# Optimization experiments

Measured on AMD Instinct MI355X. Metric: run time of the kernel, lower is better.

## Reference

```python
import jax, jax.numpy as jnp
import numpy as np

N_NODES = 100000
N_EDGES = 1600000
IN_CH, HID_CH, OUT_CH = 128, 64, 32


def setup_inputs() -> dict:
    key = jax.random.key(0)
    k1, k2, k3, k4 = jax.random.split(key, 4)
    x = jax.random.normal(k1, (N_NODES, IN_CH), dtype=jnp.float32)
    edge_index = jax.random.randint(k2, (2, N_EDGES), 0, N_NODES, dtype=jnp.int32)
    # Glorot-ish scaling like PyG's GCNConv init
    W1 = jax.random.normal(k3, (IN_CH, HID_CH), dtype=jnp.float32) / np.sqrt(IN_CH)
    b1 = jnp.zeros((HID_CH,), dtype=jnp.float32)
    W2 = jax.random.normal(k4, (HID_CH, OUT_CH), dtype=jnp.float32) / np.sqrt(HID_CH)
    b2 = jnp.zeros((OUT_CH,), dtype=jnp.float32)
    return {"x": x, "edge_index": edge_index, "W1": W1, "b1": b1, "W2": W2, "b2": b2}


def reference(x, edge_index, W1, b1, W2, b2):
    # PyG GCNConv semantics: add self-loops, symmetric deg^{-1/2} normalization,
    # linear transform, scatter-add aggregation to destination nodes, add bias.
    N = x.shape[0]
    loops = jnp.arange(N, dtype=edge_index.dtype)
    src = jnp.concatenate([edge_index[0], loops])  # [E+N]
    dst = jnp.concatenate([edge_index[1], loops])  # [E+N]

    deg = jax.ops.segment_sum(jnp.ones_like(src, dtype=x.dtype), dst, num_segments=N)
    dis = jnp.where(deg > 0, jax.lax.rsqrt(jnp.maximum(deg, 1.0)), 0.0)  # deg^{-1/2}
    norm = (dis[src] * dis[dst])[:, None]  # [E+N, 1]

    def gcn_conv(h, W, b):
        h = h @ W                                   # [N, C_out]
        msgs = h[src] * norm                        # gather + scale, [E+N, C_out]
        return jax.ops.segment_sum(msgs, dst, num_segments=N) + b

    h = jax.nn.relu(gcn_conv(x, W1, b1))
    # dropout is identity in eval mode (training=False)
    return gcn_conv(h, W2, b2)
```

## Files before the change

kernel.cpp:

```cpp
#include <hip/hip_runtime.h>
#include <hip/hip_bf16.h>

#define IN_CH 128
#define HID_CH 64
#define OUT_CH 32
#define EPB 2048
#define MAXB 512

typedef unsigned short ushort_t;
typedef __attribute__((ext_vector_type(8))) short short8;
typedef __attribute__((ext_vector_type(4))) float float4v;

static __device__ __forceinline__ ushort_t f2bf(float f) {
    unsigned u = __float_as_uint(f);
    unsigned r = (u + 0x7fff + ((u >> 16) & 1)) >> 16;
    return (ushort_t)r;
}
static __device__ __forceinline__ float bf_lo(unsigned u) { return __uint_as_float(u << 16); }
static __device__ __forceinline__ float bf_hi(unsigned u) { return __uint_as_float(u & 0xffff0000u); }


__global__ __launch_bounds__(256) void k_partition(const int* __restrict__ src,
                                                   const int* __restrict__ dst,
                                                   int* __restrict__ gcursor,
                                                   unsigned* __restrict__ pairs,
                                                   int E, int nbk, int cap) {
    __shared__ int lhist[MAXB];
    __shared__ int lbase[MAXB];
    __shared__ int lcur[MAXB];
    const int tid = threadIdx.x;
    for (int b = tid; b < nbk; b += 256) { lhist[b] = 0; lcur[b] = 0; }
    __syncthreads();
    int s[8], d[8];
    const int e0 = blockIdx.x * EPB;
#pragma unroll
    for (int j = 0; j < 8; ++j) {
        int e = e0 + j * 256 + tid;
        if (e < E) {
            s[j] = src[e];
            d[j] = dst[e];
            atomicAdd(&lhist[d[j] >> 8], 1);
        } else {
            d[j] = -1;
        }
    }
    __syncthreads();
    for (int b = tid; b < nbk; b += 256)
        lbase[b] = lhist[b] ? atomicAdd(&gcursor[b], lhist[b]) : 0;
    __syncthreads();
#pragma unroll
    for (int j = 0; j < 8; ++j) {
        if (d[j] >= 0) {
            int b = d[j] >> 8;
            int loc = atomicAdd(&lcur[b], 1);
            int idx = lbase[b] + loc;
            if (idx < cap)
                pairs[(long long)b * cap + idx] = ((unsigned)s[j] << 8) | (unsigned)(d[j] & 255);
        }
    }
}

__global__ __launch_bounds__(512) void k_bscan(const int* __restrict__ gcursor,
                                               int* __restrict__ bbase,
                                               int* __restrict__ rowptr,
                                               int nbk, int cap, int N) {
    __shared__ int s[512];
    const int tid = threadIdx.x;
    int v = (tid < nbk) ? min(gcursor[tid], cap) : 0;
    s[tid] = v;
    __syncthreads();
    for (int off = 1; off < 512; off <<= 1) {
        int val = (tid >= off) ? s[tid - off] : 0;
        __syncthreads();
        s[tid] += val;
        __syncthreads();
    }
    if (tid < nbk) bbase[tid] = s[tid] - v;
    if (tid == nbk - 1) rowptr[N] = s[tid];
}

__global__ __launch_bounds__(256) void k_bucket_build(const unsigned* __restrict__ pairs,
                                                      const int* __restrict__ gcursor,
                                                      const int* __restrict__ bbase,
                                                      int* __restrict__ rowptr,
                                                      int* __restrict__ col,
                                                      float* __restrict__ dis,
                                                      int cap, int N) {
    __shared__ int lc[256];
    __shared__ int ls[256];
    __shared__ int lcur[256];
    const int b = blockIdx.x, tid = threadIdx.x;
    lc[tid] = 0;
    __syncthreads();
    const int cnt = min(gcursor[b], cap);
    const int base = bbase[b];
    const unsigned* p = pairs + (long long)b * cap;
    for (int i = tid; i < cnt; i += 256) atomicAdd(&lc[p[i] & 255], 1);
    __syncthreads();
    const int v = lc[tid];
    ls[tid] = v;
    __syncthreads();
    for (int off = 1; off < 256; off <<= 1) {
        int val = (tid >= off) ? ls[tid - off] : 0;
        __syncthreads();
        ls[tid] += val;
        __syncthreads();
    }
    const int excl = ls[tid] - v;
    const int row = b * 256 + tid;
    if (row < N) {
        rowptr[row] = base + excl;
        dis[row] = rsqrtf((float)(v + 1));
    }
    lcur[tid] = base + excl;
    __syncthreads();
    for (int i = tid; i < cnt; i += 256) {
        unsigned pk = p[i];
        int pos = atomicAdd(&lcur[pk & 255], 1);
        col[pos] = (int)(pk >> 8);
    }
}


__global__ __launch_bounds__(256) void k_prepW(const float* __restrict__ W,
                                               unsigned* __restrict__ wsW) {
    int s = blockIdx.x * 256 + threadIdx.x;
    if (s >= 1024) return;
    int lane = s & 63;
    int nt = (s >> 6) & 3;
    int kc = s >> 8;
    int c = nt * 16 + (lane & 15);
    int k0 = kc * 32 + (lane >> 4) * 8;
    unsigned o[4];
#pragma unroll
    for (int d = 0; d < 4; ++d) {
        unsigned lo = f2bf(W[(k0 + 2 * d) * 64 + c]);
        unsigned hi = f2bf(W[(k0 + 2 * d + 1) * 64 + c]);
        o[d] = lo | (hi << 16);
    }
    ((uint4*)wsW)[s] = make_uint4(o[0], o[1], o[2], o[3]);
}


__global__ __launch_bounds__(256) void k_mm1(const float* __restrict__ X,
                                             const unsigned* __restrict__ wsW,
                                             ushort_t* __restrict__ H, int N) {
    const int tid = threadIdx.x;
    const int wv = tid >> 6, lane = tid & 63;
    const int quad = lane >> 4, n16 = lane & 15;
    const int rowbase = blockIdx.x * 64 + wv * 16;
    const int myrow = rowbase + n16;
    const bool rok = (myrow < N);

    float4v acc0 = {}, acc1 = {}, acc2 = {}, acc3 = {};

#pragma unroll
    for (int kc = 0; kc < 4; ++kc) {
        float4 xa = make_float4(0.f, 0.f, 0.f, 0.f), xb = xa;
        if (rok) {
            const float4* p = (const float4*)(X + (long long)myrow * 128 + kc * 32 + quad * 8);
            xa = p[0];
            xb = p[1];
        }
        unsigned pk[4];
        pk[0] = (unsigned)f2bf(xa.x) | ((unsigned)f2bf(xa.y) << 16);
        pk[1] = (unsigned)f2bf(xa.z) | ((unsigned)f2bf(xa.w) << 16);
        pk[2] = (unsigned)f2bf(xb.x) | ((unsigned)f2bf(xb.y) << 16);
        pk[3] = (unsigned)f2bf(xb.z) | ((unsigned)f2bf(xb.w) << 16);
        short8 a;
        a[0] = (short)(pk[0] & 0xffff); a[1] = (short)(pk[0] >> 16);
        a[2] = (short)(pk[1] & 0xffff); a[3] = (short)(pk[1] >> 16);
        a[4] = (short)(pk[2] & 0xffff); a[5] = (short)(pk[2] >> 16);
        a[6] = (short)(pk[3] & 0xffff); a[7] = (short)(pk[3] >> 16);

        const short8* wb = (const short8*)wsW;
        short8 b0 = wb[(kc * 4 + 0) * 64 + lane];
        short8 b1 = wb[(kc * 4 + 1) * 64 + lane];
        short8 b2 = wb[(kc * 4 + 2) * 64 + lane];
        short8 b3 = wb[(kc * 4 + 3) * 64 + lane];

        acc0 = __builtin_amdgcn_mfma_f32_16x16x32_bf16(a, b0, acc0, 0, 0, 0);
        acc1 = __builtin_amdgcn_mfma_f32_16x16x32_bf16(a, b1, acc1, 0, 0, 0);
        acc2 = __builtin_amdgcn_mfma_f32_16x16x32_bf16(a, b2, acc2, 0, 0, 0);
        acc3 = __builtin_amdgcn_mfma_f32_16x16x32_bf16(a, b3, acc3, 0, 0, 0);
    }

#pragma unroll
    for (int i = 0; i < 4; ++i) {
        int row = rowbase + quad * 4 + i;
        if (row < N) {
            long long o = (long long)row * 64 + n16;
            H[o]      = f2bf(acc0[i]);
            H[o + 16] = f2bf(acc1[i]);
            H[o + 32] = f2bf(acc2[i]);
            H[o + 48] = f2bf(acc3[i]);
        }
    }
}


__global__ __launch_bounds__(256) void k_mm2(const unsigned* __restrict__ Z,
                                             const float* __restrict__ W,
                                             ushort_t* __restrict__ H, int N) {
    __shared__ float sW[64 * 32];
    __shared__ float sX[64 * 64];
    const int tid = threadIdx.x;
    for (int i = tid; i < 512; i += 256) ((float4*)sW)[i] = ((const float4*)W)[i];
    const long long row0 = (long long)blockIdx.x * 64;
    for (int i = tid; i < 2048; i += 256) {
        int r = i >> 5;
        int cp = i & 31;
        long long row = row0 + r;
        unsigned u = (row < N) ? Z[row * 32 + cp] : 0u;
        sX[r * 64 + 2 * cp]     = fmaxf(bf_lo(u), 0.f);
        sX[r * 64 + 2 * cp + 1] = fmaxf(bf_hi(u), 0.f);
    }
    __syncthreads();
    const int wv = tid >> 6, lane = tid & 63;
    const int c = lane & 31, hf = lane >> 5;
    const int rbase = wv * 16 + hf * 8;
    float acc[8] = {};
#pragma unroll 2
    for (int k = 0; k < 64; k += 4) {
        float4 xv[8];
#pragma unroll
        for (int r = 0; r < 8; ++r) xv[r] = *(const float4*)&sX[(rbase + r) * 64 + k];
        float w0 = sW[k * 32 + c];
        float w1 = sW[(k + 1) * 32 + c];
        float w2 = sW[(k + 2) * 32 + c];
        float w3 = sW[(k + 3) * 32 + c];
#pragma unroll
        for (int r = 0; r < 8; ++r)
            acc[r] += xv[r].x * w0 + xv[r].y * w1 + xv[r].z * w2 + xv[r].w * w3;
    }
#pragma unroll
    for (int r = 0; r < 8; ++r) {
        long long row = row0 + rbase + r;
        if (row < N) H[row * 32 + c] = f2bf(acc[r]);
    }
}


__global__ __launch_bounds__(256) void k_agg64(const unsigned* __restrict__ h,
                                               const int* __restrict__ rowptr,
                                               const int* __restrict__ col,
                                               const float* __restrict__ dis,
                                               const float* __restrict__ b,
                                               unsigned* __restrict__ z, int N) {
    const int wave = (blockIdx.x * 256 + threadIdx.x) >> 6;
    const int lane = threadIdx.x & 63;
    if (wave >= N) return;
    const int row = wave;
    const int t = lane & 31, g = lane >> 5;
    const int start = rowptr[row];
    const int deg = rowptr[row + 1] - start;
    const float dr = dis[row];

    int myCol = row;
    float myDis = 0.f;
    if (lane < deg) {
        myCol = col[start + lane];
        myDis = dis[myCol];
    }

    unsigned us = h[row * 32 + t];
    float w0s = g ? 0.f : dr;
    float ax = w0s * bf_lo(us), ay = w0s * bf_hi(us);

    const int cnt = min(deg, 64);
    for (int k0 = 0; k0 < cnt; k0 += 8) {
#pragma unroll
        for (int u = 0; u < 4; ++u) {
            int slot = k0 + 2 * u + g;
            int s = __shfl(myCol, slot);
            float w = __shfl(myDis, slot);
            unsigned uu = h[s * 32 + t];
            ax += w * bf_lo(uu);
            ay += w * bf_hi(uu);
        }
    }
    for (int j = start + 64 + g; j < start + deg; j += 2) {
        int s = col[j];
        float w = dis[s];
        unsigned uu = h[s * 32 + t];
        ax += w * bf_lo(uu);
        ay += w * bf_hi(uu);
    }
    ax += __shfl_down(ax, 32);
    ay += __shfl_down(ay, 32);
    if (!g) {
        float2 bv = ((const float2*)b)[t];
        float ox = bv.x + dr * ax;
        float oy = bv.y + dr * ay;
        z[row * 32 + t] = (unsigned)f2bf(ox) | ((unsigned)f2bf(oy) << 16);
    }
}

__global__ __launch_bounds__(256) void k_agg32(const unsigned* __restrict__ h,
                                               const int* __restrict__ rowptr,
                                               const int* __restrict__ col,
                                               const float* __restrict__ dis,
                                               const float* __restrict__ b,
                                               float* __restrict__ out, int N) {
    const int wave = (blockIdx.x * 256 + threadIdx.x) >> 6;
    const int lane = threadIdx.x & 63;
    if (wave >= N) return;
    const int row = wave;
    const int t = lane & 15, g = lane >> 4;
    const int start = rowptr[row];
    const int deg = rowptr[row + 1] - start;
    const float dr = dis[row];

    int myCol = row;
    float myDis = 0.f;
    if (lane < deg) {
        myCol = col[start + lane];
        myDis = dis[myCol];
    }

    unsigned us = h[row * 16 + t];
    float w0s = g ? 0.f : dr;
    float ax = w0s * bf_lo(us), ay = w0s * bf_hi(us);

    const int cnt = min(deg, 64);
    for (int k0 = 0; k0 < cnt; k0 += 16) {
#pragma unroll
        for (int u = 0; u < 4; ++u) {
            int slot = k0 + 4 * u + g;
            int s = __shfl(myCol, slot);
            float w = __shfl(myDis, slot);
            unsigned uu = h[s * 16 + t];
            ax += w * bf_lo(uu);
            ay += w * bf_hi(uu);
        }
    }
    for (int j = start + 64 + g; j < start + deg; j += 4) {
        int s = col[j];
        float w = dis[s];
        unsigned uu = h[s * 16 + t];
        ax += w * bf_lo(uu);
        ay += w * bf_hi(uu);
    }
    ax += __shfl_down(ax, 32);
    ay += __shfl_down(ay, 32);
    ax += __shfl_down(ax, 16);
    ay += __shfl_down(ay, 16);
    if (!g) {
        float2 bv = ((const float2*)b)[t];
        float2 o;
        o.x = bv.x + dr * ax;
        o.y = bv.y + dr * ay;
        ((float2*)out)[row * 16 + t] = o;
    }
}

extern "C" void kernel_launch(void* const* d_in, const int* in_sizes, int n_in,
                              void* d_out, int out_size, void* d_ws, size_t ws_size,
                              hipStream_t stream) {
    const float* x  = (const float*)d_in[0];
    const int*   ei = (const int*)d_in[1];
    const float* W1 = (const float*)d_in[2];
    const float* b1 = (const float*)d_in[3];
    const float* W2 = (const float*)d_in[4];
    const float* b2 = (const float*)d_in[5];
    float* out = (float*)d_out;

    const int N = in_sizes[0] / IN_CH;
    const int E = in_sizes[1] / 2;
    const int* esrc = ei;
    const int* edst = ei + E;

    int nbk = (N + 255) >> 8;
    if (nbk > MAXB) nbk = MAXB;
    const int per_b = (E + nbk - 1) / nbk;
    const int cap = per_b + per_b / 4 + 256;

    int* rowptr   = (int*)d_ws;
    int* gcursor  = rowptr + (((N + 1) + 15) & ~15);
    int* bbase    = gcursor + MAXB;
    unsigned* wsW = (unsigned*)(bbase + MAXB);
    int* col      = (int*)(wsW + 4096);
    float* dis    = (float*)(col + ((E + 15) & ~15));
    ushort_t* h1  = (ushort_t*)(dis + ((N + 15) & ~15));
    unsigned* z1  = (unsigned*)(h1 + (((long long)N * 64 + 31) & ~31LL));
    unsigned* pairs = z1;
    ushort_t* h2  = h1;

    const int B = 256;

    hipMemsetAsync(gcursor, 0, MAXB * sizeof(int), stream);
    k_prepW<<<4, B, 0, stream>>>(W1, wsW);
    k_partition<<<(E + EPB - 1) / EPB, B, 0, stream>>>(esrc, edst, gcursor, pairs, E, nbk, cap);
    k_bscan<<<1, 512, 0, stream>>>(gcursor, bbase, rowptr, nbk, cap, N);
    k_bucket_build<<<nbk, B, 0, stream>>>(pairs, gcursor, bbase, rowptr, col, dis, cap, N);

    k_mm1<<<(N + 63) / 64, B, 0, stream>>>(x, wsW, h1, N);
    k_agg64<<<((long long)N * 64 + B - 1) / B, B, 0, stream>>>((const unsigned*)h1, rowptr, col, dis, b1, z1, N);

    k_mm2<<<(N + 63) / 64, B, 0, stream>>>(z1, W2, h2, N);
    k_agg32<<<((long long)N * 64 + B - 1) / B, B, 0, stream>>>((const unsigned*)h2, rowptr, col, dis, b2, out, N);
}
```

Before: 261.5 us.

## Fuse layer-1 aggregation with second matmul and drop separate memset

Merges the 64-channel aggregation kernel with the 64x32 matmul: each wave aggregates a row, stages it in shared memory, applies ReLU and multiplies by W2 held in registers, then writes the bf16 32-channel row. This removes the intermediate z1 write/read and one kernel launch. The gcursor memset is folded into the weight prep kernel, and the gather loops in both aggregation kernels are unrolled further. The fused kernel uses a grid-stride loop with 8 rows per wave and keeps 32 weight registers per lane, which may raise register pressure and lower occupancy for the latency-bound gather.

```diff
diff --git a/kernel.cpp b/kernel.cpp
--- a/kernel.cpp
+++ b/kernel.cpp
@@ -123,8 +123,10 @@
 
 
 __global__ __launch_bounds__(256) void k_prepW(const float* __restrict__ W,
-                                               unsigned* __restrict__ wsW) {
+                                               unsigned* __restrict__ wsW,
+                                               int* __restrict__ gcursor) {
     int s = blockIdx.x * 256 + threadIdx.x;
+    if (s < MAXB) gcursor[s] = 0;
     if (s >= 1024) return;
     int lane = s & 63;
     int nt = (s >> 6) & 3;
@@ -199,102 +201,89 @@
 }
 
 
-__global__ __launch_bounds__(256) void k_mm2(const unsigned* __restrict__ Z,
-                                             const float* __restrict__ W,
-                                             ushort_t* __restrict__ H, int N) {
-    __shared__ float sW[64 * 32];
-    __shared__ float sX[64 * 64];
-    const int tid = threadIdx.x;
-    for (int i = tid; i < 512; i += 256) ((float4*)sW)[i] = ((const float4*)W)[i];
-    const long long row0 = (long long)blockIdx.x * 64;
-    for (int i = tid; i < 2048; i += 256) {
-        int r = i >> 5;
-        int cp = i & 31;
-        long long row = row0 + r;
-        unsigned u = (row < N) ? Z[row * 32 + cp] : 0u;
-        sX[r * 64 + 2 * cp]     = fmaxf(bf_lo(u), 0.f);
-        sX[r * 64 + 2 * cp + 1] = fmaxf(bf_hi(u), 0.f);
-    }
-    __syncthreads();
-    const int wv = tid >> 6, lane = tid & 63;
-    const int c = lane & 31, hf = lane >> 5;
-    const int rbase = wv * 16 + hf * 8;
-    float acc[8] = {};
-#pragma unroll 2
-    for (int k = 0; k < 64; k += 4) {
-        float4 xv[8];
-#pragma unroll
-        for (int r = 0; r < 8; ++r) xv[r] = *(const float4*)&sX[(rbase + r) * 64 + k];
-        float w0 = sW[k * 32 + c];
-        float w1 = sW[(k + 1) * 32 + c];
-        float w2 = sW[(k + 2) * 32 + c];
-        float w3 = sW[(k + 3) * 32 + c];
-#pragma unroll
-        for (int r = 0; r < 8; ++r)
-            acc[r] += xv[r].x * w0 + xv[r].y * w1 + xv[r].z * w2 + xv[r].w * w3;
-    }
-#pragma unroll
-    for (int r = 0; r < 8; ++r) {
-        long long row = row0 + rbase + r;
-        if (row < N) H[row * 32 + c] = f2bf(acc[r]);
-    }
-}
-
-
-__global__ __launch_bounds__(256) void k_agg64(const unsigned* __restrict__ h,
-                                               const int* __restrict__ rowptr,
-                                               const int* __restrict__ col,
-                                               const float* __restrict__ dis,
-                                               const float* __restrict__ b,
-                                               unsigned* __restrict__ z, int N) {
-    const int wave = (blockIdx.x * 256 + threadIdx.x) >> 6;
-    const int lane = threadIdx.x & 63;
-    if (wave >= N) return;
-    const int row = wave;
+__global__ __launch_bounds__(256) void k_agg64_mm2(const unsigned* __restrict__ h,
+                                                   const int* __restrict__ rowptr,
+                                                   const int* __restrict__ col,
+                                                   const float* __restrict__ dis,
+                                                   const float* __restrict__ b1,
+                                                   const float* __restrict__ W2,
+                                                   unsigned* __restrict__ h2, int N) {
+    __shared__ float zbuf[4][64];
+    const int wv = threadIdx.x >> 6, lane = threadIdx.x & 63;
     const int t = lane & 31, g = lane >> 5;
-    const int start = rowptr[row];
-    const int deg = rowptr[row + 1] - start;
-    const float dr = dis[row];
-
-    int myCol = row;
-    float myDis = 0.f;
-    if (lane < deg) {
-        myCol = col[start + lane];
-        myDis = dis[myCol];
-    }
-
-    unsigned us = h[row * 32 + t];
-    float w0s = g ? 0.f : dr;
-    float ax = w0s * bf_lo(us), ay = w0s * bf_hi(us);
-
-    const int cnt = min(deg, 64);
-    for (int k0 = 0; k0 < cnt; k0 += 8) {
-#pragma unroll
-        for (int u = 0; u < 4; ++u) {
-            int slot = k0 + 2 * u + g;
-            int s = __shfl(myCol, slot);
-            float w = __shfl(myDis, slot);
+
+    float w[32];
+#pragma unroll
+    for (int k = 0; k < 32; ++k) w[k] = W2[(g * 32 + k) * 32 + t];
+    const float2 bv = ((const float2*)b1)[t];
+
+    const int wave0 = blockIdx.x * 4 + wv;
+    const int nwaves = gridDim.x * 4;
+
+    for (int row = wave0; row < N; row += nwaves) {
+        const int start = rowptr[row];
+        const int deg = rowptr[row + 1] - start;
+        const float dr = dis[row];
+
+        int myCol = row;
+        float myDis = 0.f;
+        if (lane < deg) {
+            myCol = col[start + lane];
+            myDis = dis[myCol];
+        }
+
+        unsigned us = h[row * 32 + t];
+        float w0s = g ? 0.f : dr;
+        float ax = w0s * bf_lo(us), ay = w0s * bf_hi(us);
+
+        const int cnt = min(deg, 64);
+        for (int k0 = 0; k0 < cnt; k0 += 16) {
+#pragma unroll
+            for (int u = 0; u < 8; ++u) {
+                int slot = k0 + 2 * u + g;
+                int s = __shfl(myCol, slot);
+                float ww = __shfl(myDis, slot);
+                unsigned uu = h[s * 32 + t];
+                ax += ww * bf_lo(uu);
+                ay += ww * bf_hi(uu);
+            }
+        }
+        for (int j = start + 64 + g; j < start + deg; j += 2) {
+            int s = col[j];
+            float ww = dis[s];
             unsigned uu = h[s * 32 + t];
-            ax += w * bf_lo(uu);
-            ay += w * bf_hi(uu);
-        }
-    }
-    for (int j = start + 64 + g; j < start + deg; j += 2) {
-        int s = col[j];
-        float w = dis[s];
-        unsigned uu = h[s * 32 + t];
-        ax += w * bf_lo(uu);
-        ay += w * bf_hi(uu);
-    }
-    ax += __shfl_down(ax, 32);
-    ay += __shfl_down(ay, 32);
-    if (!g) {
-        float2 bv = ((const float2*)b)[t];
-        float ox = bv.x + dr * ax;
-        float oy = bv.y + dr * ay;
-        z[row * 32 + t] = (unsigned)f2bf(ox) | ((unsigned)f2bf(oy) << 16);
-    }
-}
+            ax += ww * bf_lo(uu);
+            ay += ww * bf_hi(uu);
+        }
+        ax += __shfl_down(ax, 32);
+        ay += __shfl_down(ay, 32);
+
+        if (!g) {
+            float2 zv;
+            zv.x = bv.x + dr * ax;
+            zv.y = bv.y + dr * ay;
+            *(float2*)&zbuf[wv][2 * t] = zv;
+        }
+        __builtin_amdgcn_wave_barrier();
+
+        float acc = 0.f;
+        const float* zp = &zbuf[wv][g * 32];
+#pragma unroll
+        for (int k = 0; k < 32; k += 4) {
+            float4 zv = *(const float4*)(zp + k);
+            acc += fmaxf(zv.x, 0.f) * w[k] + fmaxf(zv.y, 0.f) * w[k + 1] +
+                   fmaxf(zv.z, 0.f) * w[k + 2] + fmaxf(zv.w, 0.f) * w[k + 3];
+        }
+        __builtin_amdgcn_wave_barrier();
+        acc += __shfl_down(acc, 32);
+
+        float o0 = __shfl(acc, 2 * t);
+        float o1 = __shfl(acc, 2 * t + 1);
+        if (lane < 16)
+            h2[row * 16 + lane] = (unsigned)f2bf(o0) | ((unsigned)f2bf(o1) << 16);
+    }
+}
+
 
 __global__ __launch_bounds__(256) void k_agg32(const unsigned* __restrict__ h,
                                                const int* __restrict__ rowptr,
@@ -319,13 +308,13 @@
     }
 
     unsigned us = h[row * 16 + t];
-    float w0s = g ? 0.f : dr;
+    float w0s = (g == 0) ? dr : 0.f;
     float ax = w0s * bf_lo(us), ay = w0s * bf_hi(us);
 
     const int cnt = min(deg, 64);
-    for (int k0 = 0; k0 < cnt; k0 += 16) {
-#pragma unroll
-        for (int u = 0; u < 4; ++u) {
+    for (int k0 = 0; k0 < cnt; k0 += 32) {
+#pragma unroll
+        for (int u = 0; u < 8; ++u) {
             int slot = k0 + 4 * u + g;
             int s = __shfl(myCol, slot);
             float w = __shfl(myDis, slot);
@@ -382,21 +371,21 @@
     int* col      = (int*)(wsW + 4096);
     float* dis    = (float*)(col + ((E + 15) & ~15));
     ushort_t* h1  = (ushort_t*)(dis + ((N + 15) & ~15));
-    unsigned* z1  = (unsigned*)(h1 + (((long long)N * 64 + 31) & ~31LL));
-    unsigned* pairs = z1;
-    ushort_t* h2  = h1;
+    unsigned* scratch = (unsigned*)(h1 + (((long long)N * 64 + 31) & ~31LL));
+    unsigned* pairs = scratch;
+    unsigned* h2    = scratch;
 
     const int B = 256;
 
-    hipMemsetAsync(gcursor, 0, MAXB * sizeof(int), stream);
-    k_prepW<<<4, B, 0, stream>>>(W1, wsW);
+    k_prepW<<<4, B, 0, stream>>>(W1, wsW, gcursor);
     k_partition<<<(E + EPB - 1) / EPB, B, 0, stream>>>(esrc, edst, gcursor, pairs, E, nbk, cap);
     k_bscan<<<1, 512, 0, stream>>>(gcursor, bbase, rowptr, nbk, cap, N);
     k_bucket_build<<<nbk, B, 0, stream>>>(pairs, gcursor, bbase, rowptr, col, dis, cap, N);
 
     k_mm1<<<(N + 63) / 64, B, 0, stream>>>(x, wsW, h1, N);
-    k_agg64<<<((long long)N * 64 + B - 1) / B, B, 0, stream>>>((const unsigned*)h1, rowptr, col, dis, b1, z1, N);
-
-    k_mm2<<<(N + 63) / 64, B, 0, stream>>>(z1, W2, h2, N);
+
+    const int fblocks = (N + 31) / 32;
+    k_agg64_mm2<<<fblocks, B, 0, stream>>>((const unsigned*)h1, rowptr, col, dis, b1, W2, h2, N);
+
     k_agg32<<<((long long)N * 64 + B - 1) / B, B, 0, stream>>>((const unsigned*)h2, rowptr, col, dis, b2, out, N);
 }
```

New measurement: 251.8 us. -3.7%, faster.
